# Performance work log

Hardware: AMD Instinct MI355X
Metric: run time of the kernel (lower is better)

The kernel has to match this reference:

```python
import jax, jax.numpy as jnp
import numpy as np

D = 64
H = 4
FF = 4  # fourier features
EPS = 1e-5


def _ln(x, g, b):
    m = jnp.mean(x, axis=-1, keepdims=True)
    v = jnp.mean((x - m) ** 2, axis=-1, keepdims=True)
    return (x - m) / jnp.sqrt(v + EPS) * g + b


def setup_inputs() -> dict:
    key = jax.random.key(0)
    ks = jax.random.split(key, 30)
    s = 0.05
    inp = {
        'feats': jax.random.normal(ks[0], (1, 1024, D), jnp.float32),
        'coors': jax.random.normal(ks[1], (1, 1024, 3), jnp.float32),
        'qkv_w': jax.random.normal(ks[2], (D, 3 * D), jnp.float32) * s,
        'out_w': jax.random.normal(ks[3], (D, D), jnp.float32) * s,
        'out_b': jnp.zeros((D,), jnp.float32),
        'edge_w1': jax.random.normal(ks[4], (2 * FF + 1, D), jnp.float32) * s,
        'edge_b1': jnp.zeros((D,), jnp.float32),
        'edge_w2': jax.random.normal(ks[5], (D, D), jnp.float32) * s,
        'edge_b2': jnp.zeros((D,), jnp.float32),
        'coord_w1': jax.random.normal(ks[6], (D, D), jnp.float32) * s,
        'coord_b1': jnp.zeros((D,), jnp.float32),
        'coord_w2': jax.random.normal(ks[7], (D, 1), jnp.float32) * s,
        'coord_b2': jnp.zeros((1,), jnp.float32),
        'gate_w1': jax.random.normal(ks[8], (D, D), jnp.float32) * s,
        'gate_b1': jnp.zeros((D,), jnp.float32),
        'gate_w2': jax.random.normal(ks[9], (D, 1), jnp.float32) * s,
        'gate_b2': jnp.zeros((1,), jnp.float32),
        'ln1_g': jnp.ones((D,), jnp.float32),
        'ln1_b': jnp.zeros((D,), jnp.float32),
        'ln2_g': jnp.ones((D,), jnp.float32),
        'ln2_b': jnp.zeros((D,), jnp.float32),
        'ffn_w1': jax.random.normal(ks[10], (D, 4 * D), jnp.float32) * s,
        'ffn_b1': jnp.zeros((4 * D,), jnp.float32),
        'ffn_w2': jax.random.normal(ks[11], (4 * D, D), jnp.float32) * s,
        'ffn_b2': jnp.zeros((D,), jnp.float32),
    }
    return inp


def reference(feats, coors, qkv_w, out_w, out_b, edge_w1, edge_b1, edge_w2, edge_b2,
              coord_w1, coord_b1, coord_w2, coord_b2, gate_w1, gate_b1, gate_w2, gate_b2,
              ln1_g, ln1_b, ln2_g, ln2_b, ffn_w1, ffn_b1, ffn_w2, ffn_b2):
    B, N, Dm = feats.shape
    x = _ln(feats, ln1_g, ln1_b)  # norm1 (pre-norm; also used as residual base, faithful to source)

    # pairwise relative coords and squared distance
    rel = coors[:, :, None, :] - coors[:, None, :, :]        # [B,N,N,3]
    rd = jnp.sum(rel ** 2, axis=-1, keepdims=True)            # [B,N,N,1]
    freqs = 2.0 ** jnp.arange(FF, dtype=coors.dtype)
    fr = rd / freqs                                           # [B,N,N,FF]
    enc = jnp.concatenate([jnp.sin(fr), jnp.cos(fr), rd], -1) # [B,N,N,2*FF+1]

    # edge MLP (edges=None, edge_dim=0)
    e_ij = jax.nn.silu(enc @ edge_w1 + edge_b1) @ edge_w2 + edge_b2  # [B,N,N,D]

    # attention
    qkv = x @ qkv_w
    q, k, v = jnp.split(qkv, 3, axis=-1)
    hd = Dm // H
    q = q.reshape(B, N, H, hd).transpose(0, 2, 1, 3)
    k = k.reshape(B, N, H, hd).transpose(0, 2, 1, 3)
    v = v.reshape(B, N, H, hd).transpose(0, 2, 1, 3)
    scores = jnp.einsum('bhid,bhjd->bhij', q, k) / jnp.sqrt(jnp.asarray(Dm, q.dtype))
    attn = jax.nn.softmax(scores, axis=-1)                    # [B,H,N,N]
    msg = jnp.einsum('bhij,bhjd->bhid', attn, v)
    msg = msg.transpose(0, 2, 1, 3).reshape(B, N, Dm)
    x = x + (msg @ out_w + out_b)
    x = x + (jax.nn.gelu(_ln(x, ln2_g, ln2_b) @ ffn_w1 + ffn_b1, approximate=False) @ ffn_w2 + ffn_b2)

    # coordinate update
    cw = (jax.nn.silu(e_ij @ coord_w1 + coord_b1) @ coord_w2 + coord_b2)[..., 0]  # [B,N,N]
    cw = cw * jnp.mean(attn, axis=1)
    gate = jax.nn.sigmoid(jax.nn.silu(x @ gate_w1 + gate_b1) @ gate_w2 + gate_b2)  # [B,N,1]
    delta = jnp.einsum('bij,bijd->bid', cw, rel) * gate
    return x, coors + delta
```

## Files before the change

kernel.cpp:

```cpp
#include <hip/hip_runtime.h>
#include <hip/hip_bf16.h>

#define N 1024
#define D 64

typedef __attribute__((ext_vector_type(8))) short bf16x8;
typedef __attribute__((ext_vector_type(4))) float f32x4;

__device__ __forceinline__ unsigned short f2b(float v) {
  unsigned u = __float_as_uint(v);
  u += 0x7fffu + ((u >> 16) & 1u);
  return (unsigned short)(u >> 16);
}
__device__ __forceinline__ unsigned short f2bc(float v) {
  union { __hip_bfloat16 h; unsigned short u; } r;
  r.h = __float2bfloat16(v);
  return r.u;
}
__device__ __forceinline__ unsigned pk2(float a, float b) {
  union { __hip_bfloat162 h; unsigned u; } r;
  r.h = __hip_bfloat162(__float2bfloat16(a), __float2bfloat16(b));
  return r.u;
}
__device__ __forceinline__ float bl(unsigned u) { return __uint_as_float(u << 16); }
__device__ __forceinline__ float bh(unsigned u) { return __uint_as_float(u & 0xffff0000u); }
__device__ __forceinline__ float silu_f(float x) {
  return x * __builtin_amdgcn_rcpf(1.f + __expf(-x));
}
__device__ __forceinline__ float sigm_f(float x) {
  return __builtin_amdgcn_rcpf(1.f + __expf(-x));
}

__global__ __launch_bounds__(64) void k_ln1_qkv(
    const float* __restrict__ feats, const float* __restrict__ g, const float* __restrict__ b,
    const float* __restrict__ qkv_w, float* __restrict__ xn, float* __restrict__ qkv) {
  const int i = blockIdx.x, t = threadIdx.x;
  float v = feats[i * D + t];
  float s = v;
#pragma unroll
  for (int off = 32; off; off >>= 1) s += __shfl_xor(s, off);
  const float m = s * (1.0f / 64.0f);
  const float dv = v - m;
  float vs = dv * dv;
#pragma unroll
  for (int off = 32; off; off >>= 1) vs += __shfl_xor(vs, off);
  const float var = vs * (1.0f / 64.0f);
  const float xv = dv * rsqrtf(var + 1e-5f) * g[t] + b[t];
  xn[i * D + t] = xv;
  __shared__ float xs[D];
  xs[t] = xv;
  __syncthreads();
#pragma unroll
  for (int c = 0; c < 3; ++c) {
    const int col = t + c * 64;
    float acc = 0.f;
#pragma unroll 8
    for (int k = 0; k < D; ++k) acc += xs[k] * qkv_w[k * 192 + col];
    qkv[i * 192 + col] = acc;
  }
}

__global__ __launch_bounds__(256) void k_scores(
    const float* __restrict__ qkv, unsigned short* __restrict__ P,
    float* __restrict__ l_ws, float* __restrict__ pv_ws) {
  const int i0 = blockIdx.x * 64, j0 = blockIdx.y * 64, jb = blockIdx.y;
  const int t = threadIdx.x;
  const int lane = t & 63, h = t >> 6;
  const int l15 = lane & 15, lg = lane >> 4;
  const int r7 = l15 & 7;

  __shared__ __align__(16) unsigned short Qs[64 * 64];
  __shared__ __align__(16) unsigned short Ks[64 * 64];
  __shared__ __align__(16) unsigned short VTs[4 * 16 * 64];
  __shared__ __align__(16) unsigned short Ps[4 * 64 * 64];

  {
    const int si = t >> 2, q4 = t & 3;
    const int g0 = ((q4 * 2) ^ (si & 7)) * 8, g1 = ((q4 * 2 + 1) ^ (si & 7)) * 8;
    {
      const float* qr = &qkv[(i0 + si) * 192 + q4 * 16];
      float4 a0 = *(const float4*)(qr + 0), a1 = *(const float4*)(qr + 4);
      float4 a2 = *(const float4*)(qr + 8), a3 = *(const float4*)(qr + 12);
      *(uint4*)&Qs[si * 64 + g0] = make_uint4(
          pk2(a0.x * 0.125f, a0.y * 0.125f), pk2(a0.z * 0.125f, a0.w * 0.125f),
          pk2(a1.x * 0.125f, a1.y * 0.125f), pk2(a1.z * 0.125f, a1.w * 0.125f));
      *(uint4*)&Qs[si * 64 + g1] = make_uint4(
          pk2(a2.x * 0.125f, a2.y * 0.125f), pk2(a2.z * 0.125f, a2.w * 0.125f),
          pk2(a3.x * 0.125f, a3.y * 0.125f), pk2(a3.z * 0.125f, a3.w * 0.125f));
    }
    {
      const float* kr = &qkv[(j0 + si) * 192 + 64 + q4 * 16];
      float4 a0 = *(const float4*)(kr + 0), a1 = *(const float4*)(kr + 4);
      float4 a2 = *(const float4*)(kr + 8), a3 = *(const float4*)(kr + 12);
      *(uint4*)&Ks[si * 64 + g0] = make_uint4(pk2(a0.x, a0.y), pk2(a0.z, a0.w),
                                              pk2(a1.x, a1.y), pk2(a1.z, a1.w));
      *(uint4*)&Ks[si * 64 + g1] = make_uint4(pk2(a2.x, a2.y), pk2(a2.z, a2.w),
                                              pk2(a3.x, a3.y), pk2(a3.z, a3.w));
    }
    {
      const float* vr = &qkv[(j0 + si) * 192 + 128 + q4 * 16];
      float4 v0 = *(const float4*)(vr + 0), v1 = *(const float4*)(vr + 4);
      float4 v2 = *(const float4*)(vr + 8), v3 = *(const float4*)(vr + 12);
      float vv[16] = {v0.x, v0.y, v0.z, v0.w, v1.x, v1.y, v1.z, v1.w,
                      v2.x, v2.y, v2.z, v2.w, v3.x, v3.y, v3.z, v3.w};
      const int sj3 = si >> 3, sj7 = si & 7;
#pragma unroll
      for (int cc = 0; cc < 16; ++cc)
        VTs[q4 * 1024 + cc * 64 + ((sj3 ^ (cc & 7)) * 8) + sj7] = f2bc(vv[cc]);
    }
  }
  __syncthreads();

  const bf16x8 z8 = {0, 0, 0, 0, 0, 0, 0, 0};
  const int gk = ((h * 2 + (lg & 1)) ^ r7) * 8;
  bf16x8 qa[4], kb[4];
#pragma unroll
  for (int it = 0; it < 4; ++it) {
    qa[it] = *(const bf16x8*)&Qs[(it * 16 + l15) * 64 + gk];
    if (lg >= 2) qa[it] = z8;
    kb[it] = *(const bf16x8*)&Ks[(it * 16 + l15) * 64 + gk];
  }
  f32x4 acc[4][4];
#pragma unroll
  for (int it = 0; it < 4; ++it)
#pragma unroll
    for (int jt = 0; jt < 4; ++jt)
      acc[it][jt] = (f32x4){0.f, 0.f, 0.f, 0.f};
#pragma unroll
  for (int it = 0; it < 4; ++it)
#pragma unroll
    for (int jt = 0; jt < 4; ++jt)
      acc[it][jt] = __builtin_amdgcn_mfma_f32_16x16x32_bf16(qa[it], kb[jt], acc[it][jt], 0, 0, 0);

  float prow[4][4];
#pragma unroll
  for (int it = 0; it < 4; ++it)
#pragma unroll
    for (int rr = 0; rr < 4; ++rr) prow[it][rr] = 0.f;
#pragma unroll
  for (int it = 0; it < 4; ++it)
#pragma unroll
    for (int jt = 0; jt < 4; ++jt)
#pragma unroll
      for (int rr = 0; rr < 4; ++rr) {
        const float p = __expf(acc[it][jt][rr]);
        prow[it][rr] += p;
        const int irow = it * 16 + lg * 4 + rr;
        const int col = jt * 16 + l15;
        Ps[h * 4096 + irow * 64 + (((col >> 3) ^ (irow & 7)) * 8) + (col & 7)] = f2bc(p);
      }
#pragma unroll
  for (int it = 0; it < 4; ++it)
#pragma unroll
    for (int rr = 0; rr < 4; ++rr) {
      float s = prow[it][rr];
      s += __shfl_xor(s, 1); s += __shfl_xor(s, 2);
      s += __shfl_xor(s, 4); s += __shfl_xor(s, 8);
      if (l15 == 0)
        l_ws[h * 16384 + jb * 1024 + i0 + it * 16 + lg * 4 + rr] = s;
    }

  f32x4 av[4];
#pragma unroll
  for (int it = 0; it < 4; ++it) av[it] = (f32x4){0.f, 0.f, 0.f, 0.f};
#pragma unroll
  for (int ks = 0; ks < 2; ++ks) {
    const int gj = ((ks * 4 + lg) ^ r7) * 8;
    bf16x8 vb = *(const bf16x8*)&VTs[h * 1024 + l15 * 64 + gj];
#pragma unroll
    for (int it = 0; it < 4; ++it) {
      bf16x8 pa = *(const bf16x8*)&Ps[h * 4096 + (it * 16 + l15) * 64 + gj];
      av[it] = __builtin_amdgcn_mfma_f32_16x16x32_bf16(pa, vb, av[it], 0, 0, 0);
    }
  }
#pragma unroll
  for (int it = 0; it < 4; ++it)
#pragma unroll
    for (int rr = 0; rr < 4; ++rr)
      pv_ws[jb * 65536 + (i0 + it * 16 + lg * 4 + rr) * 64 + h * 16 + l15] = av[it][rr];

  {
    const int ir = t & 63;
    unsigned short* pg = &P[h * 1048576 + (i0 + ir) * 1024 + j0];
#pragma unroll
    for (int gg = 0; gg < 8; ++gg)
      *(uint4*)&pg[gg * 8] = *(const uint4*)&Ps[h * 4096 + ir * 64 + ((gg ^ (ir & 7)) * 8)];
  }
}

__global__ __launch_bounds__(256) void k_lred(
    const float* __restrict__ l_ws, float* __restrict__ inv_l) {
  const int idx = blockIdx.x * 256 + threadIdx.x;
  const int h = idx >> 10, i = idx & 1023;
  float s = 0.f;
#pragma unroll
  for (int jt = 0; jt < 16; ++jt) s += l_ws[h * 16384 + jt * 1024 + i];
  inv_l[idx] = __builtin_amdgcn_rcpf(s);
}

__global__ __launch_bounds__(256) void k_meanattn(
    const unsigned short* __restrict__ P, const float* __restrict__ inv_l,
    float* __restrict__ meanattn) {
  const int i = blockIdx.x, t = threadIdx.x;
  const float w0 = 0.25f * inv_l[i], w1 = 0.25f * inv_l[1024 + i];
  const float w2 = 0.25f * inv_l[2048 + i], w3 = 0.25f * inv_l[3072 + i];
  const int j = t * 4;
  uint2 p0 = *(const uint2*)&P[i * 1024 + j];
  uint2 p1 = *(const uint2*)&P[1048576 + i * 1024 + j];
  uint2 p2 = *(const uint2*)&P[2097152 + i * 1024 + j];
  uint2 p3 = *(const uint2*)&P[3145728 + i * 1024 + j];
  float4 o;
  o.x = w0 * bl(p0.x) + w1 * bl(p1.x) + w2 * bl(p2.x) + w3 * bl(p3.x);
  o.y = w0 * bh(p0.x) + w1 * bh(p1.x) + w2 * bh(p2.x) + w3 * bh(p3.x);
  o.z = w0 * bl(p0.y) + w1 * bl(p1.y) + w2 * bl(p2.y) + w3 * bl(p3.y);
  o.w = w0 * bh(p0.y) + w1 * bh(p1.y) + w2 * bh(p2.y) + w3 * bh(p3.y);
  *(float4*)&meanattn[i * 1024 + j] = o;
}

__global__ __launch_bounds__(256) void k_ffn_gate(
    const float* __restrict__ pv_ws, const float* __restrict__ inv_l,
    const float* __restrict__ xn,
    const float* __restrict__ out_w, const float* __restrict__ out_b,
    const float* __restrict__ ln2_g, const float* __restrict__ ln2_b,
    const float* __restrict__ fw1, const float* __restrict__ fb1,
    const float* __restrict__ fw2, const float* __restrict__ fb2,
    const float* __restrict__ gw1, const float* __restrict__ gb1,
    const float* __restrict__ gw2, const float* __restrict__ gb2,
    float* __restrict__ xout, float* __restrict__ gate) {
  const int i = blockIdx.x, t = threadIdx.x;
  __shared__ float msgv[64], xs[64], x1s[64], hs[256];
  if (t < 64) {
    float s = 0.f;
#pragma unroll
    for (int jt = 0; jt < 16; ++jt) s += pv_ws[jt * 65536 + i * 64 + t];
    msgv[t] = s * inv_l[(t >> 4) * 1024 + i];
  }
  __syncthreads();
  if (t < 64) {
    float o = out_b[t];
#pragma unroll 8
    for (int k = 0; k < 64; ++k) o += msgv[k] * out_w[k * 64 + t];
    const float v = xn[i * 64 + t] + o;
    x1s[t] = v;
    float s = v;
#pragma unroll
    for (int off = 32; off; off >>= 1) s += __shfl_xor(s, off);
    const float m = s * (1.f / 64.f);
    const float dv = v - m;
    float vs = dv * dv;
#pragma unroll
    for (int off = 32; off; off >>= 1) vs += __shfl_xor(vs, off);
    xs[t] = dv * rsqrtf(vs * (1.f / 64.f) + 1e-5f) * ln2_g[t] + ln2_b[t];
  }
  __syncthreads();
  float a = fb1[t];
#pragma unroll 8
  for (int k = 0; k < 64; ++k) a += xs[k] * fw1[k * 256 + t];
  const float ge = 0.5f * a * (1.f + erff(a * 0.70710678118f));
  hs[t] = ge;
  __syncthreads();
  if (t < 64) {
    float o = fb2[t];
#pragma unroll 8
    for (int k = 0; k < 256; ++k) o += hs[k] * fw2[k * 64 + t];
    const float xo = x1s[t] + o;
    xout[i * 64 + t] = xo;
    xs[t] = xo;
  }
  __syncthreads();
  if (t < 64) {
    float a2 = gb1[t];
#pragma unroll 8
    for (int k = 0; k < 64; ++k) a2 += xs[k] * gw1[k * 64 + t];
    const float sg = a2 * sigm_f(a2);
    float pp = sg * gw2[t];
#pragma unroll
    for (int off = 32; off; off >>= 1) pp += __shfl_xor(pp, off);
    if (t == 0) gate[i] = sigm_f(pp + gb2[0]);
  }
}

__global__ __launch_bounds__(256) void k_prep(
    const float* __restrict__ ew1, const float* __restrict__ eb1,
    const float* __restrict__ ew2, const float* __restrict__ cw1,
    const float* __restrict__ eb2, const float* __restrict__ cb1,
    unsigned short* __restrict__ pw, float* __restrict__ b3p) {
  const int t = threadIdx.x;
  __shared__ float wc[64][64];
  for (int idx = t; idx < 4096; idx += 256) {
    const int r = idx >> 6, c = idx & 63;
    float s = 0.f;
#pragma unroll 8
    for (int k = 0; k < 64; ++k) s += ew2[r * 64 + k] * cw1[k * 64 + c];
    wc[r][c] = s;
  }
  __syncthreads();
  for (int idx = t; idx < 12 * 512; idx += 256) {
    const int e = idx & 7, l = (idx >> 3) & 63, f = idx >> 9;
    const int l15 = l & 15, lg = l >> 4;
    float v;
    if (f < 4) {
      const int d = f * 16 + l15, k = lg * 8 + e;
      v = (k < 9) ? ew1[k * 64 + d] : (k == 9 ? eb1[d] : 0.f);
    } else {
      const int g = f - 4, d = (g >> 1) * 16 + l15, k = (g & 1) * 32 + lg * 8 + e;
      v = wc[k][d];
    }
    pw[idx] = f2b(v);
  }
  if (t < 64) {
    float s = cb1[t];
#pragma unroll 8
    for (int k = 0; k < 64; ++k) s += eb2[k] * cw1[k * 64 + t];
    b3p[t] = s;
  }
}

__global__ __launch_bounds__(256, 2) void k_pair(
    const float* __restrict__ coors, const float* __restrict__ meanattn,
    const unsigned short* __restrict__ pw,
    const float* __restrict__ b3p, const float* __restrict__ c2g,
    const float* __restrict__ cb2, const float* __restrict__ gate,
    float* __restrict__ outc) {
  const int i = blockIdx.x;
  const int t = threadIdx.x;
  const int w = t >> 6;
  const int lane = t & 63;
  const int l15 = lane & 15;
  const int lg = lane >> 4;

  __shared__ __align__(16) unsigned short buf[4][2][32][64];
  __shared__ float4 relma[4][32];
  __shared__ float redb[4][3];

  bf16x8 wf[12];
#pragma unroll
  for (int f = 0; f < 12; ++f)
    wf[f] = *(const bf16x8*)&pw[(f * 64 + lane) * 8];

  float b3v[16], c2v[16];
#pragma unroll
  for (int mt = 0; mt < 4; ++mt)
#pragma unroll
    for (int r = 0; r < 4; ++r) {
      const int d = mt * 16 + lg * 4 + r;
      b3v[mt * 4 + r] = b3p[d];
      c2v[mt * 4 + r] = c2g[d];
    }
  const float cb2q = cb2[0] * 0.25f;
  const float cix = coors[i * 3 + 0], ciy = coors[i * 3 + 1], ciz = coors[i * 3 + 2];

  if (lane < 32) {
    const int j = lane;
    unsigned short* rp = &buf[w][0][j][0];
    const uint4 z4 = make_uint4(0, 0, 0, 0);
    *(uint4*)&rp[(1 ^ (j & 7)) * 8] = z4;
    *(uint4*)&rp[(2 ^ (j & 7)) * 8] = z4;
    *(uint4*)&rp[(3 ^ (j & 7)) * 8] = z4;
  }

  float dx = 0.f, dy = 0.f, dz = 0.f;
  f32x4 acc[4][2];

  for (int c = 0; c < 8; ++c) {
    {
      const int j = lane & 31;
      const int half = lane >> 5;
      const int jg = c * 128 + w * 32 + j;
      const float rx = cix - coors[jg * 3 + 0];
      const float ry = ciy - coors[jg * 3 + 1];
      const float rz = ciz - coors[jg * 3 + 2];
      const float rd = rx * rx + ry * ry + rz * rz;
      unsigned short* rp = &buf[w][0][j][0];
      if (half == 0) {
        const float ma = meanattn[i * N + jg];
        relma[w][j] = make_float4(ma * rx, ma * ry, ma * rz, 0.f);
        *(uint2*)&rp[(0 ^ (j & 7)) * 8] =
            make_uint2(pk2(__sinf(rd), __sinf(rd * 0.5f)),
                       pk2(__sinf(rd * 0.25f), __sinf(rd * 0.125f)));
        *(unsigned*)&rp[(1 ^ (j & 7)) * 8] = pk2(rd, 1.0f);
      } else {
        *(uint2*)&rp[((0 ^ (j & 7)) * 8) + 4] =
            make_uint2(pk2(__cosf(rd), __cosf(rd * 0.5f)),
                       pk2(__cosf(rd * 0.25f), __cosf(rd * 0.125f)));
      }
    }

#pragma unroll
    for (int mt = 0; mt < 4; ++mt)
#pragma unroll
      for (int nt = 0; nt < 2; ++nt)
        acc[mt][nt] = (f32x4){0.f, 0.f, 0.f, 0.f};
    {
      const int j0 = l15, j1 = 16 + l15;
      bf16x8 bf0 = *(const bf16x8*)&buf[w][0][j0][(lg ^ (j0 & 7)) * 8];
      bf16x8 bf1 = *(const bf16x8*)&buf[w][0][j1][(lg ^ (j1 & 7)) * 8];
#pragma unroll
      for (int mt = 0; mt < 4; ++mt) {
        acc[mt][0] = __builtin_amdgcn_mfma_f32_16x16x32_bf16(wf[mt], bf0, acc[mt][0], 0, 0, 0);
        acc[mt][1] = __builtin_amdgcn_mfma_f32_16x16x32_bf16(wf[mt], bf1, acc[mt][1], 0, 0, 0);
      }
    }
#pragma unroll
    for (int mt = 0; mt < 4; ++mt)
#pragma unroll
      for (int nt = 0; nt < 2; ++nt) {
        const f32x4 a = acc[mt][nt];
        const unsigned lo = pk2(silu_f(a[0]), silu_f(a[1]));
        const unsigned hi = pk2(silu_f(a[2]), silu_f(a[3]));
        const int j = nt * 16 + l15;
        const int g = mt * 2 + (lg >> 1);
        *(uint2*)&buf[w][1][j][((g ^ (j & 7)) * 8) + (lg & 1) * 4] = make_uint2(lo, hi);
      }

#pragma unroll
    for (int mt = 0; mt < 4; ++mt)
#pragma unroll
      for (int nt = 0; nt < 2; ++nt)
        acc[mt][nt] = (f32x4){b3v[mt * 4 + 0], b3v[mt * 4 + 1], b3v[mt * 4 + 2], b3v[mt * 4 + 3]};
#pragma unroll
    for (int ks = 0; ks < 2; ++ks) {
      const int gi = ks * 4 + lg;
      const int j0 = l15, j1 = 16 + l15;
      bf16x8 bf0 = *(const bf16x8*)&buf[w][1][j0][(gi ^ (j0 & 7)) * 8];
      bf16x8 bf1 = *(const bf16x8*)&buf[w][1][j1][(gi ^ (j1 & 7)) * 8];
#pragma unroll
      for (int mt = 0; mt < 4; ++mt) {
        acc[mt][0] = __builtin_amdgcn_mfma_f32_16x16x32_bf16(wf[4 + mt * 2 + ks], bf0, acc[mt][0], 0, 0, 0);
        acc[mt][1] = __builtin_amdgcn_mfma_f32_16x16x32_bf16(wf[4 + mt * 2 + ks], bf1, acc[mt][1], 0, 0, 0);
      }
    }

#pragma unroll
    for (int nt = 0; nt < 2; ++nt) {
      float cwp = cb2q;
#pragma unroll
      for (int mt = 0; mt < 4; ++mt) {
        const f32x4 a = acc[mt][nt];
#pragma unroll
        for (int r = 0; r < 4; ++r) cwp += silu_f(a[r]) * c2v[mt * 4 + r];
      }
      const float4 rm = relma[w][nt * 16 + l15];
      dx += cwp * rm.x;
      dy += cwp * rm.y;
      dz += cwp * rm.z;
    }
  }

#pragma unroll
  for (int off = 1; off < 64; off <<= 1) {
    dx += __shfl_xor(dx, off);
    dy += __shfl_xor(dy, off);
    dz += __shfl_xor(dz, off);
  }
  if (lane == 0) { redb[w][0] = dx; redb[w][1] = dy; redb[w][2] = dz; }
  __syncthreads();
  if (t == 0) {
    const float gg = gate[i];
    const float sx = redb[0][0] + redb[1][0] + redb[2][0] + redb[3][0];
    const float sy = redb[0][1] + redb[1][1] + redb[2][1] + redb[3][1];
    const float sz = redb[0][2] + redb[1][2] + redb[2][2] + redb[3][2];
    outc[i * 3 + 0] = cix + sx * gg;
    outc[i * 3 + 1] = ciy + sy * gg;
    outc[i * 3 + 2] = ciz + sz * gg;
  }
}

extern "C" void kernel_launch(void* const* d_in, const int* in_sizes, int n_in,
                              void* d_out, int out_size, void* d_ws, size_t ws_size,
                              hipStream_t stream) {
  const float* feats = (const float*)d_in[0];
  const float* coors = (const float*)d_in[1];
  const float* qkv_w = (const float*)d_in[2];
  const float* out_w = (const float*)d_in[3];
  const float* out_b = (const float*)d_in[4];
  const float* ew1 = (const float*)d_in[5];
  const float* eb1 = (const float*)d_in[6];
  const float* ew2 = (const float*)d_in[7];
  const float* eb2 = (const float*)d_in[8];
  const float* cw1 = (const float*)d_in[9];
  const float* cb1 = (const float*)d_in[10];
  const float* cw2 = (const float*)d_in[11];
  const float* cb2 = (const float*)d_in[12];
  const float* gw1 = (const float*)d_in[13];
  const float* gb1 = (const float*)d_in[14];
  const float* gw2 = (const float*)d_in[15];
  const float* gb2 = (const float*)d_in[16];
  const float* ln1_g = (const float*)d_in[17];
  const float* ln1_b = (const float*)d_in[18];
  const float* ln2_g = (const float*)d_in[19];
  const float* ln2_b = (const float*)d_in[20];
  const float* fw1 = (const float*)d_in[21];
  const float* fb1 = (const float*)d_in[22];
  const float* fw2 = (const float*)d_in[23];
  const float* fb2 = (const float*)d_in[24];

  float* ws = (float*)d_ws;
  float* xn = ws;
  float* qkv = ws + 65536;
  float* gate = ws + 262144;
  unsigned short* pw = (unsigned short*)(ws + 263168);
  float* b3p = ws + 267264;
  float* inv_l = ws + 267328;
  float* l_ws = ws + 271424;
  float* meanattn = ws + 336960;
  float* pv_ws = ws + 1385536;
  unsigned short* P = (unsigned short*)(ws + 2434112);

  float* xout = (float*)d_out;
  float* coorout = xout + 65536;

  hipLaunchKernelGGL(k_ln1_qkv, dim3(N), dim3(64), 0, stream, feats, ln1_g, ln1_b, qkv_w, xn, qkv);
  hipLaunchKernelGGL(k_prep, dim3(1), dim3(256), 0, stream, ew1, eb1, ew2, cw1, eb2, cb1, pw, b3p);
  hipLaunchKernelGGL(k_scores, dim3(16, 16), dim3(256), 0, stream, qkv, P, l_ws, pv_ws);
  hipLaunchKernelGGL(k_lred, dim3(16), dim3(256), 0, stream, l_ws, inv_l);
  hipLaunchKernelGGL(k_meanattn, dim3(N), dim3(256), 0, stream, P, inv_l, meanattn);
  hipLaunchKernelGGL(k_ffn_gate, dim3(N), dim3(256), 0, stream, pv_ws, inv_l, xn,
                     out_w, out_b, ln2_g, ln2_b,
                     fw1, fb1, fw2, fb2, gw1, gb1, gw2, gb2, xout, gate);
  hipLaunchKernelGGL(k_pair, dim3(N), dim3(256), 0, stream, coors, meanattn, pw,
                     b3p, cw2, cb2, gate, coorout);
}
```

Measured before the change: 110.0 us.

## Fuse softmax normalization and mean-attention into pair kernel; split pair over j halves

Removes the k_lred and k_meanattn kernels. The l-sum reduction now runs inside k_ffn_gate and k_pair, and k_pair reads bf16 P directly to build the head-averaged attention per pair. That avoids writing and rereading the 4 MB fp32 meanattn buffer. k_pair is split into two j-halves via blockIdx.y to double the grid and now writes partial sums, with a new tiny k_finalize kernel applying the gate and residual. The per-row l-sum reduction is recomputed redundantly in each block, and the scalar P loads in k_pair are 2-byte gathers across 4 heads.

```diff
diff --git a/kernel.cpp b/kernel.cpp
--- a/kernel.cpp
+++ b/kernel.cpp
@@ -22,8 +22,9 @@
   r.h = __hip_bfloat162(__float2bfloat16(a), __float2bfloat16(b));
   return r.u;
 }
-__device__ __forceinline__ float bl(unsigned u) { return __uint_as_float(u << 16); }
-__device__ __forceinline__ float bh(unsigned u) { return __uint_as_float(u & 0xffff0000u); }
+__device__ __forceinline__ float bu(unsigned short u) {
+  return __uint_as_float(((unsigned)u) << 16);
+}
 __device__ __forceinline__ float silu_f(float x) {
   return x * __builtin_amdgcn_rcpf(1.f + __expf(-x));
 }
@@ -188,37 +189,8 @@
   }
 }
 
-__global__ __launch_bounds__(256) void k_lred(
-    const float* __restrict__ l_ws, float* __restrict__ inv_l) {
-  const int idx = blockIdx.x * 256 + threadIdx.x;
-  const int h = idx >> 10, i = idx & 1023;
-  float s = 0.f;
-#pragma unroll
-  for (int jt = 0; jt < 16; ++jt) s += l_ws[h * 16384 + jt * 1024 + i];
-  inv_l[idx] = __builtin_amdgcn_rcpf(s);
-}
-
-__global__ __launch_bounds__(256) void k_meanattn(
-    const unsigned short* __restrict__ P, const float* __restrict__ inv_l,
-    float* __restrict__ meanattn) {
-  const int i = blockIdx.x, t = threadIdx.x;
-  const float w0 = 0.25f * inv_l[i], w1 = 0.25f * inv_l[1024 + i];
-  const float w2 = 0.25f * inv_l[2048 + i], w3 = 0.25f * inv_l[3072 + i];
-  const int j = t * 4;
-  uint2 p0 = *(const uint2*)&P[i * 1024 + j];
-  uint2 p1 = *(const uint2*)&P[1048576 + i * 1024 + j];
-  uint2 p2 = *(const uint2*)&P[2097152 + i * 1024 + j];
-  uint2 p3 = *(const uint2*)&P[3145728 + i * 1024 + j];
-  float4 o;
-  o.x = w0 * bl(p0.x) + w1 * bl(p1.x) + w2 * bl(p2.x) + w3 * bl(p3.x);
-  o.y = w0 * bh(p0.x) + w1 * bh(p1.x) + w2 * bh(p2.x) + w3 * bh(p3.x);
-  o.z = w0 * bl(p0.y) + w1 * bl(p1.y) + w2 * bl(p2.y) + w3 * bl(p3.y);
-  o.w = w0 * bh(p0.y) + w1 * bh(p1.y) + w2 * bh(p2.y) + w3 * bh(p3.y);
-  *(float4*)&meanattn[i * 1024 + j] = o;
-}
-
 __global__ __launch_bounds__(256) void k_ffn_gate(
-    const float* __restrict__ pv_ws, const float* __restrict__ inv_l,
+    const float* __restrict__ pv_ws, const float* __restrict__ l_ws,
     const float* __restrict__ xn,
     const float* __restrict__ out_w, const float* __restrict__ out_b,
     const float* __restrict__ ln2_g, const float* __restrict__ ln2_b,
@@ -230,10 +202,14 @@
   const int i = blockIdx.x, t = threadIdx.x;
   __shared__ float msgv[64], xs[64], x1s[64], hs[256];
   if (t < 64) {
+    float ls = 0.f;
+#pragma unroll
+    for (int jt = 0; jt < 16; ++jt) ls += l_ws[(t >> 4) * 16384 + jt * 1024 + i];
+    const float invh = __builtin_amdgcn_rcpf(ls);
     float s = 0.f;
 #pragma unroll
     for (int jt = 0; jt < 16; ++jt) s += pv_ws[jt * 65536 + i * 64 + t];
-    msgv[t] = s * inv_l[(t >> 4) * 1024 + i];
+    msgv[t] = s * invh;
   }
   __syncthreads();
   if (t < 64) {
@@ -317,21 +293,29 @@
 }
 
 __global__ __launch_bounds__(256, 2) void k_pair(
-    const float* __restrict__ coors, const float* __restrict__ meanattn,
-    const unsigned short* __restrict__ pw,
+    const float* __restrict__ coors, const unsigned short* __restrict__ P,
+    const float* __restrict__ l_ws, const unsigned short* __restrict__ pw,
     const float* __restrict__ b3p, const float* __restrict__ c2g,
-    const float* __restrict__ cb2, const float* __restrict__ gate,
-    float* __restrict__ outc) {
+    const float* __restrict__ cb2, float* __restrict__ partial) {
   const int i = blockIdx.x;
+  const int half = blockIdx.y;
   const int t = threadIdx.x;
   const int w = t >> 6;
   const int lane = t & 63;
   const int l15 = lane & 15;
   const int lg = lane >> 4;
 
-  __shared__ __align__(16) unsigned short buf[4][2][32][64];
+  __shared__ __align__(16) unsigned short buf[4][32][64];
   __shared__ float4 relma[4][32];
+  __shared__ float invl_s[4];
   __shared__ float redb[4][3];
+
+  if (t < 4) {
+    float s = 0.f;
+#pragma unroll
+    for (int jt = 0; jt < 16; ++jt) s += l_ws[t * 16384 + jt * 1024 + i];
+    invl_s[t] = 0.25f * __builtin_amdgcn_rcpf(s);
+  }
 
   bf16x8 wf[12];
 #pragma unroll
@@ -352,28 +336,33 @@
 
   if (lane < 32) {
     const int j = lane;
-    unsigned short* rp = &buf[w][0][j][0];
+    unsigned short* rp = &buf[w][j][0];
     const uint4 z4 = make_uint4(0, 0, 0, 0);
     *(uint4*)&rp[(1 ^ (j & 7)) * 8] = z4;
     *(uint4*)&rp[(2 ^ (j & 7)) * 8] = z4;
     *(uint4*)&rp[(3 ^ (j & 7)) * 8] = z4;
   }
+  __syncthreads();
 
   float dx = 0.f, dy = 0.f, dz = 0.f;
   f32x4 acc[4][2];
 
-  for (int c = 0; c < 8; ++c) {
+  for (int c = 0; c < 4; ++c) {
     {
       const int j = lane & 31;
-      const int half = lane >> 5;
-      const int jg = c * 128 + w * 32 + j;
+      const int hhalf = lane >> 5;
+      const int jg = half * 512 + c * 128 + w * 32 + j;
       const float rx = cix - coors[jg * 3 + 0];
       const float ry = ciy - coors[jg * 3 + 1];
       const float rz = ciz - coors[jg * 3 + 2];
       const float rd = rx * rx + ry * ry + rz * rz;
-      unsigned short* rp = &buf[w][0][j][0];
-      if (half == 0) {
-        const float ma = meanattn[i * N + jg];
+      unsigned short* rp = &buf[w][j][0];
+      if (hhalf == 0) {
+        const float p0 = bu(P[i * 1024 + jg]);
+        const float p1 = bu(P[1048576 + i * 1024 + jg]);
+        const float p2 = bu(P[2097152 + i * 1024 + jg]);
+        const float p3 = bu(P[3145728 + i * 1024 + jg]);
+        const float ma = p0 * invl_s[0] + p1 * invl_s[1] + p2 * invl_s[2] + p3 * invl_s[3];
         relma[w][j] = make_float4(ma * rx, ma * ry, ma * rz, 0.f);
         *(uint2*)&rp[(0 ^ (j & 7)) * 8] =
             make_uint2(pk2(__sinf(rd), __sinf(rd * 0.5f)),
@@ -393,8 +382,8 @@
         acc[mt][nt] = (f32x4){0.f, 0.f, 0.f, 0.f};
     {
       const int j0 = l15, j1 = 16 + l15;
-      bf16x8 bf0 = *(const bf16x8*)&buf[w][0][j0][(lg ^ (j0 & 7)) * 8];
-      bf16x8 bf1 = *(const bf16x8*)&buf[w][0][j1][(lg ^ (j1 & 7)) * 8];
+      bf16x8 bf0 = *(const bf16x8*)&buf[w][j0][(lg ^ (j0 & 7)) * 8];
+      bf16x8 bf1 = *(const bf16x8*)&buf[w][j1][(lg ^ (j1 & 7)) * 8];
 #pragma unroll
       for (int mt = 0; mt < 4; ++mt) {
         acc[mt][0] = __builtin_amdgcn_mfma_f32_16x16x32_bf16(wf[mt], bf0, acc[mt][0], 0, 0, 0);
@@ -410,7 +399,7 @@
         const unsigned hi = pk2(silu_f(a[2]), silu_f(a[3]));
         const int j = nt * 16 + l15;
         const int g = mt * 2 + (lg >> 1);
-        *(uint2*)&buf[w][1][j][((g ^ (j & 7)) * 8) + (lg & 1) * 4] = make_uint2(lo, hi);
+        *(uint2*)&buf[w][j][((g ^ (j & 7)) * 8) + (lg & 1) * 4] = make_uint2(lo, hi);
       }
 
 #pragma unroll
@@ -422,8 +411,8 @@
     for (int ks = 0; ks < 2; ++ks) {
       const int gi = ks * 4 + lg;
       const int j0 = l15, j1 = 16 + l15;
-      bf16x8 bf0 = *(const bf16x8*)&buf[w][1][j0][(gi ^ (j0 & 7)) * 8];
-      bf16x8 bf1 = *(const bf16x8*)&buf[w][1][j1][(gi ^ (j1 & 7)) * 8];
+      bf16x8 bf0 = *(const bf16x8*)&buf[w][j0][(gi ^ (j0 & 7)) * 8];
+      bf16x8 bf1 = *(const bf16x8*)&buf[w][j1][(gi ^ (j1 & 7)) * 8];
 #pragma unroll
       for (int mt = 0; mt < 4; ++mt) {
         acc[mt][0] = __builtin_amdgcn_mfma_f32_16x16x32_bf16(wf[4 + mt * 2 + ks], bf0, acc[mt][0], 0, 0, 0);
@@ -456,13 +445,22 @@
   if (lane == 0) { redb[w][0] = dx; redb[w][1] = dy; redb[w][2] = dz; }
   __syncthreads();
   if (t == 0) {
-    const float gg = gate[i];
-    const float sx = redb[0][0] + redb[1][0] + redb[2][0] + redb[3][0];
-    const float sy = redb[0][1] + redb[1][1] + redb[2][1] + redb[3][1];
-    const float sz = redb[0][2] + redb[1][2] + redb[2][2] + redb[3][2];
-    outc[i * 3 + 0] = cix + sx * gg;
-    outc[i * 3 + 1] = ciy + sy * gg;
-    outc[i * 3 + 2] = ciz + sz * gg;
+    const int o = (i * 2 + half) * 3;
+    partial[o + 0] = redb[0][0] + redb[1][0] + redb[2][0] + redb[3][0];
+    partial[o + 1] = redb[0][1] + redb[1][1] + redb[2][1] + redb[3][1];
+    partial[o + 2] = redb[0][2] + redb[1][2] + redb[2][2] + redb[3][2];
+  }
+}
+
+__global__ __launch_bounds__(256) void k_finalize(
+    const float* __restrict__ coors, const float* __restrict__ partial,
+    const float* __restrict__ gate, float* __restrict__ outc) {
+  const int i = blockIdx.x * 256 + threadIdx.x;
+  if (i < N) {
+    const float g = gate[i];
+#pragma unroll
+    for (int c = 0; c < 3; ++c)
+      outc[i * 3 + c] = coors[i * 3 + c] + (partial[i * 6 + c] + partial[i * 6 + 3 + c]) * g;
   }
 }
 
@@ -501,11 +499,10 @@
   float* gate = ws + 262144;
   unsigned short* pw = (unsigned short*)(ws + 263168);
   float* b3p = ws + 267264;
-  float* inv_l = ws + 267328;
-  float* l_ws = ws + 271424;
-  float* meanattn = ws + 336960;
-  float* pv_ws = ws + 1385536;
-  unsigned short* P = (unsigned short*)(ws + 2434112);
+  float* l_ws = ws + 267328;
+  float* pv_ws = ws + 332864;
+  float* partial = ws + 1381440;
+  unsigned short* P = (unsigned short*)(ws + 1387584);
 
   float* xout = (float*)d_out;
   float* coorout = xout + 65536;
@@ -513,11 +510,10 @@
   hipLaunchKernelGGL(k_ln1_qkv, dim3(N), dim3(64), 0, stream, feats, ln1_g, ln1_b, qkv_w, xn, qkv);
   hipLaunchKernelGGL(k_prep, dim3(1), dim3(256), 0, stream, ew1, eb1, ew2, cw1, eb2, cb1, pw, b3p);
   hipLaunchKernelGGL(k_scores, dim3(16, 16), dim3(256), 0, stream, qkv, P, l_ws, pv_ws);
-  hipLaunchKernelGGL(k_lred, dim3(16), dim3(256), 0, stream, l_ws, inv_l);
-  hipLaunchKernelGGL(k_meanattn, dim3(N), dim3(256), 0, stream, P, inv_l, meanattn);
-  hipLaunchKernelGGL(k_ffn_gate, dim3(N), dim3(256), 0, stream, pv_ws, inv_l, xn,
+  hipLaunchKernelGGL(k_ffn_gate, dim3(N), dim3(256), 0, stream, pv_ws, l_ws, xn,
                      out_w, out_b, ln2_g, ln2_b,
                      fw1, fb1, fw2, fb2, gw1, gb1, gw2, gb2, xout, gate);
-  hipLaunchKernelGGL(k_pair, dim3(N), dim3(256), 0, stream, coors, meanattn, pw,
-                     b3p, cw2, cb2, gate, coorout);
-}
+  hipLaunchKernelGGL(k_pair, dim3(N, 2), dim3(256), 0, stream, coors, P, l_ws, pw,
+                     b3p, cw2, cb2, partial);
+  hipLaunchKernelGGL(k_finalize, dim3(4), dim3(256), 0, stream, coors, partial, gate, coorout);
+}
```

Result: no change. 109.3 us (-0.6%).
